# Performance work log

Hardware: AMD Instinct MI355X
Metric: run time of the kernel (lower is better)

Reference implementation:

```python
import jax, jax.numpy as jnp
import numpy as np

N = 4096
NEG_SLOPE = 0.2


def _gat_layer(x, src, dst, W, Wb, a, ab):
    # h = Linear(x); e_ij = a([h_i, h_j]) for each edge; dense softmax over dim=1; ELU
    h = x @ W + Wb                               # [N, D]
    D = h.shape[-1]
    e = h[src] @ a[:D] + h[dst] @ a[D:] + ab     # [E] per-edge attention logits
    n = x.shape[0]
    attn = jnp.full((n, n), -jnp.inf, dtype=x.dtype).at[src, dst].set(e)
    attn = jnp.where(attn > 0, attn, NEG_SLOPE * attn)   # leaky_relu (keeps -inf)
    attn = jax.nn.softmax(attn, axis=1)
    return jax.nn.elu(attn @ h)                  # sigma = ELU


def _multihead(x, src, dst, hW, hWb, ha, hab, oW, oWb, oa, oab):
    # concat=False: mean over head outputs, then out GATLayer
    heads = jax.vmap(lambda W, Wb, a, ab: _gat_layer(x, src, dst, W, Wb, a, ab))(hW, hWb, ha, hab)
    xm = heads.mean(axis=0)
    return _gat_layer(xm, src, dst, oW, oWb, oa, oab)


def setup_inputs() -> dict:
    key = jax.random.key(0)
    ks = jax.random.split(key, 20)
    in_dim, hid, out_dim, H, E = 512, 256, 128, 4, 131072
    x = jax.random.normal(ks[0], (N, in_dim), jnp.float32)
    edge_index = jax.random.randint(ks[1], (2, E), 0, N)
    # force self loops so every softmax row has at least one finite entry
    edge_index = edge_index.at[:, :N].set(jnp.broadcast_to(jnp.arange(N), (2, N)))

    def lin(k, shape, fan_in):
        return jax.random.uniform(k, shape, jnp.float32, -1.0, 1.0) / np.sqrt(fan_in).astype(np.float32)

    return {
        "x": x,
        "edge_index": edge_index,
        # layer 0 (MultiHeadGAT in_dim->hid)
        "l0_hW": lin(ks[2], (H, in_dim, hid), in_dim),
        "l0_hWb": lin(ks[3], (H, hid), in_dim),
        "l0_ha": lin(ks[4], (H, 2 * hid), 2 * hid),
        "l0_hab": lin(ks[5], (H,), 2 * hid),
        "l0_oW": lin(ks[6], (hid, hid), hid),
        "l0_oWb": lin(ks[7], (hid,), hid),
        "l0_oa": lin(ks[8], (2 * hid,), 2 * hid),
        "l0_oab": lin(ks[9], (), 2 * hid),
        # layer 1 (MultiHeadGAT hid->hid)
        "l1_hW": lin(ks[10], (H, hid, hid), hid),
        "l1_hWb": lin(ks[11], (H, hid), hid),
        "l1_ha": lin(ks[12], (H, 2 * hid), 2 * hid),
        "l1_hab": lin(ks[13], (H,), 2 * hid),
        "l1_oW": lin(ks[14], (hid, hid), hid),
        "l1_oWb": lin(ks[15], (hid,), hid),
        "l1_oa": lin(ks[16], (2 * hid,), 2 * hid),
        "l1_oab": lin(ks[17], (), 2 * hid),
        # final Linear(hid -> out_dim)
        "lin_W": lin(ks[18], (hid, out_dim), hid),
        "lin_b": lin(ks[19], (out_dim,), hid),
    }


def reference(x, edge_index, l0_hW, l0_hWb, l0_ha, l0_hab, l0_oW, l0_oWb, l0_oa, l0_oab,
              l1_hW, l1_hWb, l1_ha, l1_hab, l1_oW, l1_oWb, l1_oa, l1_oab, lin_W, lin_b):
    src, dst = edge_index[0], edge_index[1]
    lrelu = lambda v: jnp.where(v > 0, v, NEG_SLOPE * v)
    h = lrelu(_multihead(x, src, dst, l0_hW, l0_hWb, l0_ha, l0_hab, l0_oW, l0_oWb, l0_oa, l0_oab))
    h = lrelu(_multihead(h, src, dst, l1_hW, l1_hWb, l1_ha, l1_hab, l1_oW, l1_oWb, l1_oa, l1_oab))
    return h @ lin_W + lin_b  # [N, out_dim], flatten(1) is a no-op for 2D
```

## Files before the change

kernel.cpp:

```cpp
#include <hip/hip_runtime.h>
#include <hip/hip_bf16.h>
#include <math.h>

#define NEG_SLOPE 0.2f

constexpr int D = 256;
constexpr int HEADS = 4;
constexpr int MAXB = 128;

typedef __attribute__((ext_vector_type(8))) short short8;
typedef __attribute__((ext_vector_type(4))) float floatx4;

__device__ inline unsigned short bf16_hi_trunc(float v) {
  return (unsigned short)(__float_as_uint(v) >> 16);
}
__device__ inline float bf16_tof(unsigned short u) {
  return __uint_as_float(((unsigned int)u) << 16);
}
__device__ inline unsigned short bf16_rn(float v) {
  unsigned int b = __float_as_uint(v);
  b += 0x7fffu + ((b >> 16) & 1u);
  return (unsigned short)(b >> 16);
}
__device__ inline void split2(float v, unsigned short& hi, unsigned short& lo) {
  hi = bf16_hi_trunc(v);
  lo = bf16_rn(v - bf16_tof(hi));
}

__global__ void fill_kernel(const int* __restrict__ src, const int* __restrict__ dst,
                            int* __restrict__ cnt, int* __restrict__ colb, int E) {
  int k = blockIdx.x * blockDim.x + threadIdx.x;
  if (k < E) {
    int s = src[k];
    int pos = atomicAdd(&cnt[s], 1);
    if (pos < MAXB) colb[s * MAXB + pos] = dst[k];
  }
}

__global__ __launch_bounds__(128) void dedupe_kernel(const int* __restrict__ cnt,
                                                     int* __restrict__ colb, int Nn) {
  __shared__ int cs[MAXB];
  int i = blockIdx.x;
  int len = cnt[i];
  if (len > MAXB) len = MAXB;
  int tid = threadIdx.x;
  if (tid < len) cs[tid] = colb[i * MAXB + tid];
  __syncthreads();
  if (tid < len) {
    int c = cs[tid];
    bool dup = false;
    for (int s2 = 0; s2 < tid; ++s2)
      if (cs[s2] == c) { dup = true; break; }
    if (dup) colb[i * MAXB + tid] = -1;
  }
}

__global__ __launch_bounds__(256) void prep_kernel(
    int* __restrict__ zeroBase, int zeroN,
    const float* __restrict__ x, unsigned short* __restrict__ xhi, unsigned short* __restrict__ xlo,
    int xN4,
    const float* __restrict__ l0hW, unsigned short* __restrict__ l0hHi, unsigned short* __restrict__ l0hLo,
    const float* __restrict__ l1hW, unsigned short* __restrict__ l1hHi, unsigned short* __restrict__ l1hLo,
    const float* __restrict__ l0oW, unsigned short* __restrict__ l0oHi, unsigned short* __restrict__ l0oLo,
    const float* __restrict__ l1oW, unsigned short* __restrict__ l1oHi, unsigned short* __restrict__ l1oLo,
    const float* __restrict__ linW, unsigned short* __restrict__ linHi, unsigned short* __restrict__ linLo) {
  const int b = blockIdx.x;
  const int t = threadIdx.x;
  if (b < 528) {
    int idx = b * 256 + t;
    if (idx < zeroN) zeroBase[idx] = 0;
    return;
  }
  if (b < 2576) {
    int idx = (b - 528) * 256 + t;
    if (idx < xN4) {
      float4 v = ((const float4*)x)[idx];
      ushort4 h, l;
      split2(v.x, h.x, l.x);
      split2(v.y, h.y, l.y);
      split2(v.z, h.z, l.z);
      split2(v.w, h.w, l.w);
      ((ushort4*)xhi)[idx] = h;
      ((ushort4*)xlo)[idx] = l;
    }
    return;
  }
  __shared__ float tile[32][33];
  const int tr = t >> 5, tc = t & 31;
  if (b < 3088) {
    const int bi = b - 2576;
    const int kb = bi & 15;
    const int nb = (bi >> 4) & 7;
    const int h = bi >> 7;
    const int K = 512, N = 256;
    const int k0 = kb * 32, n0 = nb * 32;
    const float* B = l0hW + (size_t)h * K * N;
#pragma unroll
    for (int i = 0; i < 4; ++i)
      tile[tr + 8 * i][tc] = B[(size_t)(k0 + tr + 8 * i) * N + (n0 + tc)];
    __syncthreads();
    unsigned short* Thi = l0hHi + (size_t)h * N * K;
    unsigned short* Tlo = l0hLo + (size_t)h * N * K;
#pragma unroll
    for (int i = 0; i < 4; ++i) {
      int n = n0 + tr + 8 * i, k = k0 + tc;
      float v = tile[tc][tr + 8 * i];
      unsigned short hi, lo;
      split2(v, hi, lo);
      Thi[(size_t)n * K + k] = hi;
      Tlo[(size_t)n * K + k] = lo;
    }
    return;
  }
  const int bi = b - 3088;
  const int kb = bi & 7;
  const int nb = (bi >> 3) & 7;
  const int z = bi >> 6;
  const int K = 256;
  const int N = (z == 6) ? 128 : 256;
  const int k0 = kb * 32, n0 = nb * 32;
  if (n0 >= N) return;
  const float* B;
  unsigned short *Thi, *Tlo;
  if (z < 4) {
    B = l1hW + (size_t)z * K * 256;
    Thi = l1hHi + (size_t)z * 256 * K;
    Tlo = l1hLo + (size_t)z * 256 * K;
  } else if (z == 4) { B = l0oW; Thi = l0oHi; Tlo = l0oLo; }
  else if (z == 5)   { B = l1oW; Thi = l1oHi; Tlo = l1oLo; }
  else               { B = linW; Thi = linHi; Tlo = linLo; }
#pragma unroll
  for (int i = 0; i < 4; ++i)
    tile[tr + 8 * i][tc] = B[(size_t)(k0 + tr + 8 * i) * N + (n0 + tc)];
  __syncthreads();
#pragma unroll
  for (int i = 0; i < 4; ++i) {
    int n = n0 + tr + 8 * i, k = k0 + tc;
    float v = tile[tc][tr + 8 * i];
    unsigned short hi, lo;
    split2(v, hi, lo);
    Thi[(size_t)n * K + k] = hi;
    Tlo[(size_t)n * K + k] = lo;
  }
}

__global__ __launch_bounds__(256) void gemm_mfma_split(
    const unsigned short* __restrict__ Ahi, const unsigned short* __restrict__ Alo,
    const unsigned short* __restrict__ Ahsep, size_t planeStride,
    const unsigned short* __restrict__ Bthi, const unsigned short* __restrict__ Btlo,
    const float* __restrict__ bias, float* __restrict__ C, unsigned short* __restrict__ Cb,
    const float* __restrict__ aptr, float* __restrict__ alphaB, float* __restrict__ betaB,
    int M, int N, int K) {
  constexpr int LSTR = 72;
  __shared__ unsigned short sA[2][64 * LSTR];
  __shared__ unsigned short sB[2][64 * LSTR];
  const int tid = threadIdx.x;
  const int bm = blockIdx.x * 64;
  const int gn = blockIdx.y * 64;
  const int head = (gn) / N;
  const int bn = gn - head * N;

  const int lane = tid & 63;
  const int wv = tid >> 6;
  const int wm = (wv & 1) * 32;
  const int wn = (wv >> 1) * 32;
  const int q = lane >> 4;
  const int l15 = lane & 15;

  floatx4 acc[2][2];
#pragma unroll
  for (int i = 0; i < 2; ++i)
#pragma unroll
    for (int j = 0; j < 2; ++j) acc[i][j] = (floatx4)0.0f;

  for (int k0 = 0; k0 < K; k0 += 64) {
    short8 ra[2][2], rb[2][2];
#pragma unroll
    for (int i = 0; i < 2; ++i) {
      const int c = tid + 256 * i;
      const int row = c >> 3, koff = (c & 7) << 3;
      const size_t boff = (size_t)(gn + row) * K + k0 + koff;
      rb[0][i] = *(const short8*)(Bthi + boff);
      rb[1][i] = *(const short8*)(Btlo + boff);
      if (Ahsep) {
        const size_t aoff = (size_t)(bm + row) * K + k0 + koff;
        const short8 u0 = *(const short8*)(Ahsep + aoff);
        const short8 u1 = *(const short8*)(Ahsep + planeStride + aoff);
        const short8 u2 = *(const short8*)(Ahsep + 2 * planeStride + aoff);
        const short8 u3 = *(const short8*)(Ahsep + 3 * planeStride + aoff);
#pragma unroll
        for (int e = 0; e < 8; ++e) {
          float f = 0.25f * (bf16_tof((unsigned short)u0[e]) + bf16_tof((unsigned short)u1[e]) +
                             bf16_tof((unsigned short)u2[e]) + bf16_tof((unsigned short)u3[e]));
          unsigned short hi, lo;
          split2(f, hi, lo);
          ra[0][i][e] = (short)hi;
          ra[1][i][e] = (short)lo;
        }
      } else {
        const size_t aoff = (size_t)(bm + row) * K + k0 + koff;
        ra[0][i] = *(const short8*)(Ahi + aoff);
        ra[1][i] = *(const short8*)(Alo + aoff);
      }
    }
    __syncthreads();
#pragma unroll
    for (int i = 0; i < 2; ++i) {
      const int c = tid + 256 * i;
      const int row = c >> 3, koff = (c & 7) << 3;
      *(short8*)(&sA[0][row * LSTR + koff]) = ra[0][i];
      *(short8*)(&sA[1][row * LSTR + koff]) = ra[1][i];
      *(short8*)(&sB[0][row * LSTR + koff]) = rb[0][i];
      *(short8*)(&sB[1][row * LSTR + koff]) = rb[1][i];
    }
    __syncthreads();
#pragma unroll
    for (int kc = 0; kc < 2; ++kc) {
      const int ko = kc * 32 + q * 8;
      short8 aH[2], aL[2], bH[2], bL[2];
#pragma unroll
      for (int i = 0; i < 2; ++i) {
        aH[i] = *(const short8*)(&sA[0][(wm + i * 16 + l15) * LSTR + ko]);
        aL[i] = *(const short8*)(&sA[1][(wm + i * 16 + l15) * LSTR + ko]);
        bH[i] = *(const short8*)(&sB[0][(wn + i * 16 + l15) * LSTR + ko]);
        bL[i] = *(const short8*)(&sB[1][(wn + i * 16 + l15) * LSTR + ko]);
      }
#pragma unroll
      for (int i = 0; i < 2; ++i)
#pragma unroll
        for (int j = 0; j < 2; ++j) {
          acc[i][j] = __builtin_amdgcn_mfma_f32_16x16x32_bf16(aH[i], bH[j], acc[i][j], 0, 0, 0);
          acc[i][j] = __builtin_amdgcn_mfma_f32_16x16x32_bf16(aH[i], bL[j], acc[i][j], 0, 0, 0);
          acc[i][j] = __builtin_amdgcn_mfma_f32_16x16x32_bf16(aL[i], bH[j], acc[i][j], 0, 0, 0);
        }
    }
  }
  const size_t cBase = (size_t)head * M * N;
  const int colh0 = bn + wn + l15;
  const int colh1 = colh0 + 16;
  const float bv0 = bias[head * N + colh0];
  const float bv1 = bias[head * N + colh1];
  float as0 = 0.f, as1 = 0.f, ad0 = 0.f, ad1 = 0.f;
  if (aptr) {
    as0 = aptr[head * 2 * N + colh0];
    as1 = aptr[head * 2 * N + colh1];
    ad0 = aptr[head * 2 * N + N + colh0];
    ad1 = aptr[head * 2 * N + N + colh1];
  }
#pragma unroll
  for (int i = 0; i < 2; ++i) {
    const int rowb = bm + wm + i * 16 + q * 4;
#pragma unroll
    for (int r = 0; r < 4; ++r) {
      const float o0 = acc[i][0][r] + bv0;
      const float o1 = acc[i][1][r] + bv1;
      if (Cb) {
        Cb[cBase + (size_t)(rowb + r) * N + colh0] = bf16_rn(o0);
        Cb[cBase + (size_t)(rowb + r) * N + colh1] = bf16_rn(o1);
      } else {
        C[cBase + (size_t)(rowb + r) * N + colh0] = o0;
        C[cBase + (size_t)(rowb + r) * N + colh1] = o1;
      }
      if (aptr) {
        float pa = o0 * as0 + o1 * as1;
        float pb = o0 * ad0 + o1 * ad1;
#pragma unroll
        for (int off = 1; off < 16; off <<= 1) {
          pa += __shfl_xor(pa, off, 64);
          pb += __shfl_xor(pb, off, 64);
        }
        if (l15 == 0) {
          atomicAdd(&alphaB[head * M + rowb + r], pa);
          atomicAdd(&betaB[head * M + rowb + r], pb);
        }
      }
    }
  }
}

__global__ __launch_bounds__(256) void gemm_bias(
    const float* __restrict__ A, const float* __restrict__ B,
    const float* __restrict__ bias, float* __restrict__ C,
    int M, int N, int K) {
  __shared__ float As[16][68];
  __shared__ float Bs[16][68];
  const int tid = threadIdx.x;
  const int bm = blockIdx.x * 64;
  const int gn = blockIdx.y * 64;
  const int head = gn / N;
  const int bn = gn - head * N;
  const float* Bh = B + (size_t)head * K * N;

  const int tx = tid & 15;
  const int ty = tid >> 4;
  const int am = tid >> 2;
  const int ak = (tid & 3) << 2;
  const int bk = tid >> 4;
  const int bn4 = (tid & 15) << 2;

  float acc[4][4] = {};

  for (int k0 = 0; k0 < K; k0 += 16) {
    float4 av = *(const float4*)(A + (size_t)(bm + am) * K + (k0 + ak));
    float4 bv = *(const float4*)(Bh + (size_t)(k0 + bk) * N + (bn + bn4));
    __syncthreads();
    As[ak + 0][am] = av.x;
    As[ak + 1][am] = av.y;
    As[ak + 2][am] = av.z;
    As[ak + 3][am] = av.w;
    *(float4*)(&Bs[bk][bn4]) = bv;
    __syncthreads();
#pragma unroll
    for (int k = 0; k < 16; ++k) {
      float4 aa = *(const float4*)(&As[k][ty << 2]);
      float4 bb = *(const float4*)(&Bs[k][tx << 2]);
      acc[0][0] += aa.x * bb.x; acc[0][1] += aa.x * bb.y; acc[0][2] += aa.x * bb.z; acc[0][3] += aa.x * bb.w;
      acc[1][0] += aa.y * bb.x; acc[1][1] += aa.y * bb.y; acc[1][2] += aa.y * bb.z; acc[1][3] += aa.y * bb.w;
      acc[2][0] += aa.z * bb.x; acc[2][1] += aa.z * bb.y; acc[2][2] += aa.z * bb.z; acc[2][3] += aa.z * bb.w;
      acc[3][0] += aa.w * bb.x; acc[3][1] += aa.w * bb.y; acc[3][2] += aa.w * bb.z; acc[3][3] += aa.w * bb.w;
    }
  }
  float* Ch = C + (size_t)head * M * N;
  const float* bh = bias + (size_t)head * N;
  const int ccol = bn + (tx << 2);
  float4 bias4 = *(const float4*)(bh + ccol);
#pragma unroll
  for (int r = 0; r < 4; ++r) {
    int row = bm + (ty << 2) + r;
    float4 o;
    o.x = acc[r][0] + bias4.x;
    o.y = acc[r][1] + bias4.y;
    o.z = acc[r][2] + bias4.z;
    o.w = acc[r][3] + bias4.w;
    *(float4*)(Ch + (size_t)row * N + ccol) = o;
  }
}

__global__ __launch_bounds__(256) void alphabeta_kernel(
    const float* __restrict__ h, const float* __restrict__ a,
    float* __restrict__ alpha, float* __restrict__ beta, int Nn) {
  __shared__ float reda[4], redb[4];
  const int i = blockIdx.x;
  const int hh = blockIdx.y;
  const int tid = threadIdx.x;
  const int lane = tid & 63, wid = tid >> 6;
  float v = h[((size_t)hh * Nn + i) * D + tid];
  float pa = v * a[hh * 2 * D + tid];
  float pb = v * a[hh * 2 * D + D + tid];
#pragma unroll
  for (int off = 32; off > 0; off >>= 1) {
    pa += __shfl_xor(pa, off, 64);
    pb += __shfl_xor(pb, off, 64);
  }
  if (lane == 0) { reda[wid] = pa; redb[wid] = pb; }
  __syncthreads();
  if (tid == 0) {
    alpha[hh * Nn + i] = reda[0] + reda[1] + reda[2] + reda[3];
    beta[hh * Nn + i] = redb[0] + redb[1] + redb[2] + redb[3];
  }
}

template <int BF16H>
__global__ __launch_bounds__(256) void attn2(
    const float* __restrict__ h, const unsigned short* __restrict__ hB,
    const float* __restrict__ alpha, const float* __restrict__ beta,
    const float* __restrict__ ab, const int* __restrict__ cnt,
    const int* __restrict__ colb, float* __restrict__ out,
    unsigned short* __restrict__ oHi, unsigned short* __restrict__ oLo,
    int Nn, int H, int mode) {
  const int tid = threadIdx.x;
  const int lane = tid & 63;
  const int wv = tid >> 6;
  const int bx = blockIdx.x;
  const int head = bx % H;
  const int rowblk = bx / H;
  const int i = rowblk * 4 + wv;

  const float* hL = BF16H ? nullptr : (h + (size_t)head * Nn * D + (lane << 2));
  const unsigned short* hLB = BF16H ? (hB + (size_t)head * Nn * D + (lane << 2)) : nullptr;
  const float* betaH = beta + (size_t)head * Nn;
  const float ai = alpha[head * Nn + i] + ab[head];
  const int start = i * MAXB;
  int len = cnt[i];
  if (len > MAXB) len = MAXB;

  float m = -3.0e38f, s = 0.0f;
  float4 acc0 = make_float4(0.0f, 0.0f, 0.0f, 0.0f);
  float4 acc1 = make_float4(0.0f, 0.0f, 0.0f, 0.0f);

  for (int t0 = 0; t0 < len; t0 += 64) {
    const int t = t0 + lane;
    const int c = (t < len) ? colb[start + t] : -1;
    float e = -3.0e38f;
    if (c >= 0) {
      e = ai + betaH[c];
      e = e > 0.0f ? e : NEG_SLOPE * e;
    }
    float cm = e;
#pragma unroll
    for (int off = 32; off > 0; off >>= 1) cm = fmaxf(cm, __shfl_xor(cm, off, 64));
    const float newm = fmaxf(m, cm);
    const float scale = __expf(m - newm);
    const float w = (c >= 0) ? __expf(e - newm) : 0.0f;
    float cs = w;
#pragma unroll
    for (int off = 32; off > 0; off >>= 1) cs += __shfl_xor(cs, off, 64);
    s = s * scale + cs;
    acc0.x *= scale; acc0.y *= scale; acc0.z *= scale; acc0.w *= scale;
    acc1.x *= scale; acc1.y *= scale; acc1.z *= scale; acc1.w *= scale;
    m = newm;

    const int cS = (c >= 0) ? c : 0;
    const int cnt2 = min(64, len - t0);
    int j = 0;
    if constexpr (BF16H) {
      for (; j + 4 <= cnt2; j += 4) {
        const int c0 = __shfl(cS, j);     const float w0 = __shfl(w, j);
        const int c1 = __shfl(cS, j + 1); const float w1 = __shfl(w, j + 1);
        const int c2 = __shfl(cS, j + 2); const float w2 = __shfl(w, j + 2);
        const int c3 = __shfl(cS, j + 3); const float w3 = __shfl(w, j + 3);
        const ushort4 u0 = *(const ushort4*)(hLB + (size_t)c0 * D);
        const ushort4 u1 = *(const ushort4*)(hLB + (size_t)c1 * D);
        const ushort4 u2 = *(const ushort4*)(hLB + (size_t)c2 * D);
        const ushort4 u3 = *(const ushort4*)(hLB + (size_t)c3 * D);
        acc0.x += w0 * bf16_tof(u0.x); acc0.y += w0 * bf16_tof(u0.y);
        acc0.z += w0 * bf16_tof(u0.z); acc0.w += w0 * bf16_tof(u0.w);
        acc1.x += w1 * bf16_tof(u1.x); acc1.y += w1 * bf16_tof(u1.y);
        acc1.z += w1 * bf16_tof(u1.z); acc1.w += w1 * bf16_tof(u1.w);
        acc0.x += w2 * bf16_tof(u2.x); acc0.y += w2 * bf16_tof(u2.y);
        acc0.z += w2 * bf16_tof(u2.z); acc0.w += w2 * bf16_tof(u2.w);
        acc1.x += w3 * bf16_tof(u3.x); acc1.y += w3 * bf16_tof(u3.y);
        acc1.z += w3 * bf16_tof(u3.z); acc1.w += w3 * bf16_tof(u3.w);
      }
      for (; j < cnt2; ++j) {
        const int cj = __shfl(cS, j);
        const float wj = __shfl(w, j);
        const ushort4 u = *(const ushort4*)(hLB + (size_t)cj * D);
        acc0.x += wj * bf16_tof(u.x); acc0.y += wj * bf16_tof(u.y);
        acc0.z += wj * bf16_tof(u.z); acc0.w += wj * bf16_tof(u.w);
      }
    } else {
      for (; j + 4 <= cnt2; j += 4) {
        const int c0 = __shfl(cS, j);     const float w0 = __shfl(w, j);
        const int c1 = __shfl(cS, j + 1); const float w1 = __shfl(w, j + 1);
        const int c2 = __shfl(cS, j + 2); const float w2 = __shfl(w, j + 2);
        const int c3 = __shfl(cS, j + 3); const float w3 = __shfl(w, j + 3);
        const float4 h0 = *(const float4*)(hL + (size_t)c0 * D);
        const float4 h1 = *(const float4*)(hL + (size_t)c1 * D);
        const float4 h2 = *(const float4*)(hL + (size_t)c2 * D);
        const float4 h3 = *(const float4*)(hL + (size_t)c3 * D);
        acc0.x += w0 * h0.x; acc0.y += w0 * h0.y; acc0.z += w0 * h0.z; acc0.w += w0 * h0.w;
        acc1.x += w1 * h1.x; acc1.y += w1 * h1.y; acc1.z += w1 * h1.z; acc1.w += w1 * h1.w;
        acc0.x += w2 * h2.x; acc0.y += w2 * h2.y; acc0.z += w2 * h2.z; acc0.w += w2 * h2.w;
        acc1.x += w3 * h3.x; acc1.y += w3 * h3.y; acc1.z += w3 * h3.z; acc1.w += w3 * h3.w;
      }
      for (; j < cnt2; ++j) {
        const int cj = __shfl(cS, j);
        const float wj = __shfl(w, j);
        const float4 hv = *(const float4*)(hL + (size_t)cj * D);
        acc0.x += wj * hv.x; acc0.y += wj * hv.y;
        acc0.z += wj * hv.z; acc0.w += wj * hv.w;
      }
    }
  }

  const float inv = 1.0f / s;
  float4 v;
  v.x = (acc0.x + acc1.x) * inv; v.y = (acc0.y + acc1.y) * inv;
  v.z = (acc0.z + acc1.z) * inv; v.w = (acc0.w + acc1.w) * inv;
  v.x = v.x > 0.0f ? v.x : expm1f(v.x);
  v.y = v.y > 0.0f ? v.y : expm1f(v.y);
  v.z = v.z > 0.0f ? v.z : expm1f(v.z);
  v.w = v.w > 0.0f ? v.w : expm1f(v.w);

  if (mode == 1 || mode == 3) {
    v.x = v.x > 0.0f ? v.x : NEG_SLOPE * v.x;
    v.y = v.y > 0.0f ? v.y : NEG_SLOPE * v.y;
    v.z = v.z > 0.0f ? v.z : NEG_SLOPE * v.z;
    v.w = v.w > 0.0f ? v.w : NEG_SLOPE * v.w;
    if (mode == 1) {
      *(float4*)(out + (size_t)i * D + (lane << 2)) = v;
    } else {
      ushort4 h4, l4;
      split2(v.x, h4.x, l4.x);
      split2(v.y, h4.y, l4.y);
      split2(v.z, h4.z, l4.z);
      split2(v.w, h4.w, l4.w);
      const size_t q4 = ((size_t)i * D >> 2) + lane;
      ((ushort4*)oHi)[q4] = h4;
      ((ushort4*)oLo)[q4] = l4;
    }
  } else if (mode == 0) {
    if constexpr (BF16H) {
      ushort4 h4;
      h4.x = bf16_rn(v.x);
      h4.y = bf16_rn(v.y);
      h4.z = bf16_rn(v.z);
      h4.w = bf16_rn(v.w);
      const size_t q4 = (((size_t)head * Nn + i) * D >> 2) + lane;
      ((ushort4*)oHi)[q4] = h4;
    } else {
      *(float4*)(out + ((size_t)head * Nn + i) * D + (lane << 2)) = v;
    }
  } else {
    const float invH = 1.0f / (float)H;
    float* o = out + (size_t)i * D + (lane << 2);
    atomicAdd(o + 0, invH * v.x);
    atomicAdd(o + 1, invH * v.y);
    atomicAdd(o + 2, invH * v.z);
    atomicAdd(o + 3, invH * v.w);
  }
}

__global__ __launch_bounds__(256) void mean4_kernel(
    float* __restrict__ hsep, int total4) {
  int idx = blockIdx.x * blockDim.x + threadIdx.x;
  if (idx < total4) {
    float4* p = (float4*)hsep;
    float4 a = p[idx], b = p[idx + total4], c = p[idx + 2 * total4], d = p[idx + 3 * total4];
    float4 o;
    o.x = 0.25f * (a.x + b.x + c.x + d.x);
    o.y = 0.25f * (a.y + b.y + c.y + d.y);
    o.z = 0.25f * (a.z + b.z + c.z + d.z);
    o.w = 0.25f * (a.w + b.w + c.w + d.w);
    p[idx] = o;
  }
}

__global__ void zero_ints(int* __restrict__ p, int n) {
  int i = blockIdx.x * blockDim.x + threadIdx.x;
  if (i < n) p[i] = 0;
}

__global__ void zero_floats(float* __restrict__ p, int n) {
  int i = blockIdx.x * blockDim.x + threadIdx.x;
  if (i < n) p[i] = 0.0f;
}

extern "C" void kernel_launch(void* const* d_in, const int* in_sizes, int n_in,
                              void* d_out, int out_size, void* d_ws, size_t ws_size,
                              hipStream_t stream) {
  const float* x = (const float*)d_in[0];
  const int* eidx = (const int*)d_in[1];
  const float* l0_hW = (const float*)d_in[2];
  const float* l0_hWb = (const float*)d_in[3];
  const float* l0_ha = (const float*)d_in[4];
  const float* l0_hab = (const float*)d_in[5];
  const float* l0_oW = (const float*)d_in[6];
  const float* l0_oWb = (const float*)d_in[7];
  const float* l0_oa = (const float*)d_in[8];
  const float* l0_oab = (const float*)d_in[9];
  const float* l1_hW = (const float*)d_in[10];
  const float* l1_hWb = (const float*)d_in[11];
  const float* l1_ha = (const float*)d_in[12];
  const float* l1_hab = (const float*)d_in[13];
  const float* l1_oW = (const float*)d_in[14];
  const float* l1_oWb = (const float*)d_in[15];
  const float* l1_oa = (const float*)d_in[16];
  const float* l1_oab = (const float*)d_in[17];
  const float* lin_W = (const float*)d_in[18];
  const float* lin_b = (const float*)d_in[19];

  const int in_dim = 512;
  const int Nn = in_sizes[0] / in_dim;
  const int E = in_sizes[1] / 2;
  const int out_dim = 128;

  char* wsp = (char*)d_ws;
  auto alloc = [&](size_t bytes) {
    char* p = wsp;
    wsp += (bytes + 255) & ~(size_t)255;
    return p;
  };
  const size_t ndBytes = sizeof(float) * (size_t)Nn * D;
  const size_t mfmaNeed = 52000000;
  const bool mfma = ws_size >= mfmaNeed;

  if (mfma) {
    unsigned short* hbufB = (unsigned short*)alloc((size_t)HEADS * Nn * D * 2);
    unsigned short* houtB = (unsigned short*)alloc((size_t)Nn * D * 2);
    unsigned short* hsepB = (unsigned short*)alloc((size_t)HEADS * Nn * D * 2);
    unsigned short* xhi  = (unsigned short*)alloc((size_t)Nn * in_dim * 2);
    unsigned short* xlo  = (unsigned short*)alloc((size_t)Nn * in_dim * 2);
    unsigned short* x1hi = xhi;
    unsigned short* x1lo = xlo;
    unsigned short* l0hHi = (unsigned short*)alloc((size_t)HEADS * in_dim * D * 2);
    unsigned short* l0hLo = (unsigned short*)alloc((size_t)HEADS * in_dim * D * 2);
    unsigned short* l1hHi = (unsigned short*)alloc((size_t)HEADS * D * D * 2);
    unsigned short* l1hLo = (unsigned short*)alloc((size_t)HEADS * D * D * 2);
    unsigned short* l0oHi = (unsigned short*)alloc((size_t)D * D * 2);
    unsigned short* l0oLo = (unsigned short*)alloc((size_t)D * D * 2);
    unsigned short* l1oHi = (unsigned short*)alloc((size_t)D * D * 2);
    unsigned short* l1oLo = (unsigned short*)alloc((size_t)D * D * 2);
    unsigned short* linHi = (unsigned short*)alloc((size_t)D * out_dim * 2);
    unsigned short* linLo = (unsigned short*)alloc((size_t)D * out_dim * 2);
    int* cnt     = (int*)alloc(sizeof(int) * Nn);
    float* abz   = (float*)alloc(sizeof(float) * 4 * 2 * HEADS * (size_t)Nn);
    int* colb    = (int*)alloc(sizeof(int) * (size_t)Nn * MAXB);
    auto alphaS = [&](int s) { return abz + (size_t)s * 2 * HEADS * Nn; };
    auto betaS  = [&](int s) { return abz + (size_t)s * 2 * HEADS * Nn + HEADS * Nn; };

    const int* src = eidx;
    const int* dst = eidx + E;

    const int zeroN = Nn + 4 * 2 * HEADS * Nn;
    prep_kernel<<<3536, 256, 0, stream>>>(
        cnt, zeroN,
        x, xhi, xlo, Nn * in_dim / 4,
        l0_hW, l0hHi, l0hLo, l1_hW, l1hHi, l1hLo,
        l0_oW, l0oHi, l0oLo, l1_oW, l1oHi, l1oLo, lin_W, linHi, linLo);

    fill_kernel<<<(E + 255) / 256, 256, 0, stream>>>(src, dst, cnt, colb, E);
    dedupe_kernel<<<Nn, 128, 0, stream>>>(cnt, colb, Nn);

    const size_t pStride = (size_t)Nn * D;

    gemm_mfma_split<<<dim3(Nn / 64, HEADS * D / 64), 256, 0, stream>>>(
        xhi, xlo, nullptr, 0, l0hHi, l0hLo, l0_hWb, nullptr, hbufB,
        l0_ha, alphaS(0), betaS(0), Nn, D, in_dim);
    attn2<1><<<HEADS * (Nn / 4), 256, 0, stream>>>(nullptr, hbufB, alphaS(0), betaS(0), l0_hab,
                                                   cnt, colb, nullptr, hsepB, nullptr, Nn, HEADS, 0);
    gemm_mfma_split<<<dim3(Nn / 64, D / 64), 256, 0, stream>>>(
        nullptr, nullptr, hsepB, pStride, l0oHi, l0oLo, l0_oWb, nullptr, houtB,
        l0_oa, alphaS(1), betaS(1), Nn, D, D);
    attn2<1><<<Nn / 4, 256, 0, stream>>>(nullptr, houtB, alphaS(1), betaS(1), l0_oab,
                                         cnt, colb, nullptr, x1hi, x1lo, Nn, 1, 3);

    gemm_mfma_split<<<dim3(Nn / 64, HEADS * D / 64), 256, 0, stream>>>(
        x1hi, x1lo, nullptr, 0, l1hHi, l1hLo, l1_hWb, nullptr, hbufB,
        l1_ha, alphaS(2), betaS(2), Nn, D, D);
    attn2<1><<<HEADS * (Nn / 4), 256, 0, stream>>>(nullptr, hbufB, alphaS(2), betaS(2), l1_hab,
                                                   cnt, colb, nullptr, hsepB, nullptr, Nn, HEADS, 0);
    gemm_mfma_split<<<dim3(Nn / 64, D / 64), 256, 0, stream>>>(
        nullptr, nullptr, hsepB, pStride, l1oHi, l1oLo, l1_oWb, nullptr, houtB,
        l1_oa, alphaS(3), betaS(3), Nn, D, D);
    attn2<1><<<Nn / 4, 256, 0, stream>>>(nullptr, houtB, alphaS(3), betaS(3), l1_oab,
                                         cnt, colb, nullptr, x1hi, x1lo, Nn, 1, 3);

    gemm_mfma_split<<<dim3(Nn / 64, out_dim / 64), 256, 0, stream>>>(
        x1hi, x1lo, nullptr, 0, linHi, linLo, lin_b, (float*)d_out, nullptr,
        nullptr, nullptr, nullptr, Nn, out_dim, D);
    return;
  }

  const size_t smallBytes = sizeof(float) * 2 * HEADS * (size_t)Nn + sizeof(int) * (Nn + (size_t)Nn * MAXB) + 4096;
  const bool staged = ws_size >= (8 * ndBytes + 2 * ndBytes + smallBytes + 65536);

  float* hbuf  = (float*)alloc(ndBytes * HEADS);
  float* hsep  = staged ? (float*)alloc(ndBytes * HEADS) : nullptr;
  float* xm    = staged ? hsep : (float*)alloc(ndBytes);
  float* x1    = (float*)alloc(ndBytes);
  float* hout  = (float*)alloc(ndBytes);
  float* alpha = (float*)alloc(sizeof(float) * HEADS * (size_t)Nn);
  float* beta  = (float*)alloc(sizeof(float) * HEADS * (size_t)Nn);
  int* cnt     = (int*)alloc(sizeof(int) * Nn);
  int* colb    = (int*)alloc(sizeof(int) * (size_t)Nn * MAXB);

  const int* src = eidx;
  const int* dst = eidx + E;

  zero_ints<<<(Nn + 255) / 256, 256, 0, stream>>>(cnt, Nn);
  fill_kernel<<<(E + 255) / 256, 256, 0, stream>>>(src, dst, cnt, colb, E);
  dedupe_kernel<<<Nn, 128, 0, stream>>>(cnt, colb, Nn);

  const int total4 = Nn * D / 4;
  const int meanBlocks = (total4 + 255) / 256;

  gemm_bias<<<dim3(Nn / 64, HEADS * D / 64), 256, 0, stream>>>(x, l0_hW, l0_hWb, hbuf, Nn, D, in_dim);
  alphabeta_kernel<<<dim3(Nn, HEADS), 256, 0, stream>>>(hbuf, l0_ha, alpha, beta, Nn);
  if (staged) {
    attn2<0><<<HEADS * (Nn / 4), 256, 0, stream>>>(hbuf, nullptr, alpha, beta, l0_hab, cnt, colb, hsep, nullptr, nullptr, Nn, HEADS, 0);
    mean4_kernel<<<meanBlocks, 256, 0, stream>>>(hsep, total4);
  } else {
    zero_floats<<<(Nn * D + 255) / 256, 256, 0, stream>>>(xm, Nn * D);
    attn2<0><<<HEADS * (Nn / 4), 256, 0, stream>>>(hbuf, nullptr, alpha, beta, l0_hab, cnt, colb, xm, nullptr, nullptr, Nn, HEADS, 2);
  }
  gemm_bias<<<dim3(Nn / 64, D / 64), 256, 0, stream>>>(xm, l0_oW, l0_oWb, hout, Nn, D, D);
  alphabeta_kernel<<<dim3(Nn, 1), 256, 0, stream>>>(hout, l0_oa, alpha, beta, Nn);
  attn2<0><<<Nn / 4, 256, 0, stream>>>(hout, nullptr, alpha, beta, l0_oab, cnt, colb, x1, nullptr, nullptr, Nn, 1, 1);

  gemm_bias<<<dim3(Nn / 64, HEADS * D / 64), 256, 0, stream>>>(x1, l1_hW, l1_hWb, hbuf, Nn, D, D);
  alphabeta_kernel<<<dim3(Nn, HEADS), 256, 0, stream>>>(hbuf, l1_ha, alpha, beta, Nn);
  if (staged) {
    attn2<0><<<HEADS * (Nn / 4), 256, 0, stream>>>(hbuf, nullptr, alpha, beta, l1_hab, cnt, colb, hsep, nullptr, nullptr, Nn, HEADS, 0);
    mean4_kernel<<<meanBlocks, 256, 0, stream>>>(hsep, total4);
  } else {
    zero_floats<<<(Nn * D + 255) / 256, 256, 0, stream>>>(xm, Nn * D);
    attn2<0><<<HEADS * (Nn / 4), 256, 0, stream>>>(hbuf, nullptr, alpha, beta, l1_hab, cnt, colb, xm, nullptr, nullptr, Nn, HEADS, 2);
  }
  gemm_bias<<<dim3(Nn / 64, D / 64), 256, 0, stream>>>(xm, l1_oW, l1_oWb, hout, Nn, D, D);
  alphabeta_kernel<<<dim3(Nn, 1), 256, 0, stream>>>(hout, l1_oa, alpha, beta, Nn);
  attn2<0><<<Nn / 4, 256, 0, stream>>>(hout, nullptr, alpha, beta, l1_oab, cnt, colb, x1, nullptr, nullptr, Nn, 1, 1);

  gemm_bias<<<dim3(Nn / 64, out_dim / 64), 256, 0, stream>>>(x1, lin_W, lin_b, (float*)d_out, Nn, out_dim, D);
}
```

Baseline: 252.4 us.

## Fuse four-head attention aggregation with head-mean into one kernel using interleaved layout

Changes the head GEMM output to a node-major interleaved layout ([N, H, D]) with alpha/beta stored per node across heads. A new attn4 kernel handles all four heads per node in one pass: it loads each neighbor's four head rows together, runs an online softmax per head, applies ELU, averages the heads and writes the hi/lo split result directly. This removes the per-head separate output buffer and the 4-plane mean-and-split work inside the following GEMM's A-load, and shares neighbor index and beta loads across heads. The cost is more registers per thread in attn4 and a fixed dependence on HEADS being 4.

```diff
diff --git a/kernel.cpp b/kernel.cpp
--- a/kernel.cpp
+++ b/kernel.cpp
@@ -146,7 +146,6 @@
 
 __global__ __launch_bounds__(256) void gemm_mfma_split(
     const unsigned short* __restrict__ Ahi, const unsigned short* __restrict__ Alo,
-    const unsigned short* __restrict__ Ahsep, size_t planeStride,
     const unsigned short* __restrict__ Bthi, const unsigned short* __restrict__ Btlo,
     const float* __restrict__ bias, float* __restrict__ C, unsigned short* __restrict__ Cb,
     const float* __restrict__ aptr, float* __restrict__ alphaB, float* __restrict__ betaB,
@@ -159,6 +158,7 @@
   const int gn = blockIdx.y * 64;
   const int head = (gn) / N;
   const int bn = gn - head * N;
+  const int Htot = (int)((gridDim.y * 64) / N);
 
   const int lane = tid & 63;
   const int wv = tid >> 6;
@@ -182,26 +182,9 @@
       const size_t boff = (size_t)(gn + row) * K + k0 + koff;
       rb[0][i] = *(const short8*)(Bthi + boff);
       rb[1][i] = *(const short8*)(Btlo + boff);
-      if (Ahsep) {
-        const size_t aoff = (size_t)(bm + row) * K + k0 + koff;
-        const short8 u0 = *(const short8*)(Ahsep + aoff);
-        const short8 u1 = *(const short8*)(Ahsep + planeStride + aoff);
-        const short8 u2 = *(const short8*)(Ahsep + 2 * planeStride + aoff);
-        const short8 u3 = *(const short8*)(Ahsep + 3 * planeStride + aoff);
-#pragma unroll
-        for (int e = 0; e < 8; ++e) {
-          float f = 0.25f * (bf16_tof((unsigned short)u0[e]) + bf16_tof((unsigned short)u1[e]) +
-                             bf16_tof((unsigned short)u2[e]) + bf16_tof((unsigned short)u3[e]));
-          unsigned short hi, lo;
-          split2(f, hi, lo);
-          ra[0][i][e] = (short)hi;
-          ra[1][i][e] = (short)lo;
-        }
-      } else {
-        const size_t aoff = (size_t)(bm + row) * K + k0 + koff;
-        ra[0][i] = *(const short8*)(Ahi + aoff);
-        ra[1][i] = *(const short8*)(Alo + aoff);
-      }
+      const size_t aoff = (size_t)(bm + row) * K + k0 + koff;
+      ra[0][i] = *(const short8*)(Ahi + aoff);
+      ra[1][i] = *(const short8*)(Alo + aoff);
     }
     __syncthreads();
 #pragma unroll
@@ -235,7 +218,8 @@
         }
     }
   }
-  const size_t cBase = (size_t)head * M * N;
+  const size_t rowStride = (size_t)Htot * N;
+  const size_t headOff = (size_t)head * N;
   const int colh0 = bn + wn + l15;
   const int colh1 = colh0 + 16;
   const float bv0 = bias[head * N + colh0];
@@ -255,11 +239,11 @@
       const float o0 = acc[i][0][r] + bv0;
       const float o1 = acc[i][1][r] + bv1;
       if (Cb) {
-        Cb[cBase + (size_t)(rowb + r) * N + colh0] = bf16_rn(o0);
-        Cb[cBase + (size_t)(rowb + r) * N + colh1] = bf16_rn(o1);
+        Cb[(size_t)(rowb + r) * rowStride + headOff + colh0] = bf16_rn(o0);
+        Cb[(size_t)(rowb + r) * rowStride + headOff + colh1] = bf16_rn(o1);
       } else {
-        C[cBase + (size_t)(rowb + r) * N + colh0] = o0;
-        C[cBase + (size_t)(rowb + r) * N + colh1] = o1;
+        C[(size_t)(rowb + r) * N + colh0] = o0;
+        C[(size_t)(rowb + r) * N + colh1] = o1;
       }
       if (aptr) {
         float pa = o0 * as0 + o1 * as1;
@@ -270,8 +254,8 @@
           pb += __shfl_xor(pb, off, 64);
         }
         if (l15 == 0) {
-          atomicAdd(&alphaB[head * M + rowb + r], pa);
-          atomicAdd(&betaB[head * M + rowb + r], pb);
+          atomicAdd(&alphaB[(size_t)(rowb + r) * Htot + head], pa);
+          atomicAdd(&betaB[(size_t)(rowb + r) * Htot + head], pb);
         }
       }
     }
@@ -358,6 +342,152 @@
     alpha[hh * Nn + i] = reda[0] + reda[1] + reda[2] + reda[3];
     beta[hh * Nn + i] = redb[0] + redb[1] + redb[2] + redb[3];
   }
+}
+
+__global__ __launch_bounds__(256) void attn4(
+    const unsigned short* __restrict__ hB,
+    const float* __restrict__ alpha, const float* __restrict__ beta,
+    const float* __restrict__ ab, const int* __restrict__ cnt,
+    const int* __restrict__ colb,
+    unsigned short* __restrict__ oHi, unsigned short* __restrict__ oLo, int Nn) {
+  const int tid = threadIdx.x;
+  const int lane = tid & 63;
+  const int wv = tid >> 6;
+  const int i = blockIdx.x * 4 + wv;
+
+  const unsigned short* hL = hB + (lane << 2);
+  const float ai0 = alpha[i * HEADS + 0] + ab[0];
+  const float ai1 = alpha[i * HEADS + 1] + ab[1];
+  const float ai2 = alpha[i * HEADS + 2] + ab[2];
+  const float ai3 = alpha[i * HEADS + 3] + ab[3];
+  const int start = i * MAXB;
+  int len = cnt[i];
+  if (len > MAXB) len = MAXB;
+
+  float m0 = -3.0e38f, m1 = -3.0e38f, m2 = -3.0e38f, m3 = -3.0e38f;
+  float s0 = 0.f, s1 = 0.f, s2 = 0.f, s3 = 0.f;
+  float4 A0 = make_float4(0.f, 0.f, 0.f, 0.f);
+  float4 A1 = make_float4(0.f, 0.f, 0.f, 0.f);
+  float4 A2 = make_float4(0.f, 0.f, 0.f, 0.f);
+  float4 A3 = make_float4(0.f, 0.f, 0.f, 0.f);
+
+  for (int t0 = 0; t0 < len; t0 += 64) {
+    const int t = t0 + lane;
+    const int c = (t < len) ? colb[start + t] : -1;
+    float e0 = -3.0e38f, e1 = -3.0e38f, e2 = -3.0e38f, e3 = -3.0e38f;
+    if (c >= 0) {
+      const float4 b4 = *(const float4*)(beta + (size_t)c * HEADS);
+      e0 = ai0 + b4.x; e1 = ai1 + b4.y; e2 = ai2 + b4.z; e3 = ai3 + b4.w;
+      e0 = e0 > 0.0f ? e0 : NEG_SLOPE * e0;
+      e1 = e1 > 0.0f ? e1 : NEG_SLOPE * e1;
+      e2 = e2 > 0.0f ? e2 : NEG_SLOPE * e2;
+      e3 = e3 > 0.0f ? e3 : NEG_SLOPE * e3;
+    }
+    float c0 = e0, c1 = e1, c2 = e2, c3 = e3;
+#pragma unroll
+    for (int off = 32; off > 0; off >>= 1) {
+      c0 = fmaxf(c0, __shfl_xor(c0, off, 64));
+      c1 = fmaxf(c1, __shfl_xor(c1, off, 64));
+      c2 = fmaxf(c2, __shfl_xor(c2, off, 64));
+      c3 = fmaxf(c3, __shfl_xor(c3, off, 64));
+    }
+    const float n0 = fmaxf(m0, c0), n1 = fmaxf(m1, c1);
+    const float n2 = fmaxf(m2, c2), n3 = fmaxf(m3, c3);
+    const float sc0 = __expf(m0 - n0), sc1 = __expf(m1 - n1);
+    const float sc2 = __expf(m2 - n2), sc3 = __expf(m3 - n3);
+    float w0 = 0.f, w1 = 0.f, w2 = 0.f, w3 = 0.f;
+    if (c >= 0) {
+      w0 = __expf(e0 - n0); w1 = __expf(e1 - n1);
+      w2 = __expf(e2 - n2); w3 = __expf(e3 - n3);
+    }
+    float q0 = w0, q1 = w1, q2 = w2, q3 = w3;
+#pragma unroll
+    for (int off = 32; off > 0; off >>= 1) {
+      q0 += __shfl_xor(q0, off, 64);
+      q1 += __shfl_xor(q1, off, 64);
+      q2 += __shfl_xor(q2, off, 64);
+      q3 += __shfl_xor(q3, off, 64);
+    }
+    s0 = s0 * sc0 + q0; s1 = s1 * sc1 + q1;
+    s2 = s2 * sc2 + q2; s3 = s3 * sc3 + q3;
+    A0.x *= sc0; A0.y *= sc0; A0.z *= sc0; A0.w *= sc0;
+    A1.x *= sc1; A1.y *= sc1; A1.z *= sc1; A1.w *= sc1;
+    A2.x *= sc2; A2.y *= sc2; A2.z *= sc2; A2.w *= sc2;
+    A3.x *= sc3; A3.y *= sc3; A3.z *= sc3; A3.w *= sc3;
+    m0 = n0; m1 = n1; m2 = n2; m3 = n3;
+
+    const int cS = (c >= 0) ? c : 0;
+    const int cnt2 = min(64, len - t0);
+    int j = 0;
+    for (; j + 2 <= cnt2; j += 2) {
+      const int ca = __shfl(cS, j);
+      const int cb = __shfl(cS, j + 1);
+      const float wa0 = __shfl(w0, j),     wa1 = __shfl(w1, j);
+      const float wa2 = __shfl(w2, j),     wa3 = __shfl(w3, j);
+      const float wb0 = __shfl(w0, j + 1), wb1 = __shfl(w1, j + 1);
+      const float wb2 = __shfl(w2, j + 1), wb3 = __shfl(w3, j + 1);
+      const unsigned short* pa = hL + (size_t)ca * (HEADS * D);
+      const unsigned short* pb = hL + (size_t)cb * (HEADS * D);
+      const ushort4 ua0 = *(const ushort4*)(pa);
+      const ushort4 ua1 = *(const ushort4*)(pa + D);
+      const ushort4 ua2 = *(const ushort4*)(pa + 2 * D);
+      const ushort4 ua3 = *(const ushort4*)(pa + 3 * D);
+      const ushort4 ub0 = *(const ushort4*)(pb);
+      const ushort4 ub1 = *(const ushort4*)(pb + D);
+      const ushort4 ub2 = *(const ushort4*)(pb + 2 * D);
+      const ushort4 ub3 = *(const ushort4*)(pb + 3 * D);
+      A0.x += wa0 * bf16_tof(ua0.x); A0.y += wa0 * bf16_tof(ua0.y);
+      A0.z += wa0 * bf16_tof(ua0.z); A0.w += wa0 * bf16_tof(ua0.w);
+      A1.x += wa1 * bf16_tof(ua1.x); A1.y += wa1 * bf16_tof(ua1.y);
+      A1.z += wa1 * bf16_tof(ua1.z); A1.w += wa1 * bf16_tof(ua1.w);
+      A2.x += wa2 * bf16_tof(ua2.x); A2.y += wa2 * bf16_tof(ua2.y);
+      A2.z += wa2 * bf16_tof(ua2.z); A2.w += wa2 * bf16_tof(ua2.w);
+      A3.x += wa3 * bf16_tof(ua3.x); A3.y += wa3 * bf16_tof(ua3.y);
+      A3.z += wa3 * bf16_tof(ua3.z); A3.w += wa3 * bf16_tof(ua3.w);
+      A0.x += wb0 * bf16_tof(ub0.x); A0.y += wb0 * bf16_tof(ub0.y);
+      A0.z += wb0 * bf16_tof(ub0.z); A0.w += wb0 * bf16_tof(ub0.w);
+      A1.x += wb1 * bf16_tof(ub1.x); A1.y += wb1 * bf16_tof(ub1.y);
+      A1.z += wb1 * bf16_tof(ub1.z); A1.w += wb1 * bf16_tof(ub1.w);
+      A2.x += wb2 * bf16_tof(ub2.x); A2.y += wb2 * bf16_tof(ub2.y);
+      A2.z += wb2 * bf16_tof(ub2.z); A2.w += wb2 * bf16_tof(ub2.w);
+      A3.x += wb3 * bf16_tof(ub3.x); A3.y += wb3 * bf16_tof(ub3.y);
+      A3.z += wb3 * bf16_tof(ub3.z); A3.w += wb3 * bf16_tof(ub3.w);
+    }
+    for (; j < cnt2; ++j) {
+      const int ca = __shfl(cS, j);
+      const float wa0 = __shfl(w0, j), wa1 = __shfl(w1, j);
+      const float wa2 = __shfl(w2, j), wa3 = __shfl(w3, j);
+      const unsigned short* pa = hL + (size_t)ca * (HEADS * D);
+      const ushort4 ua0 = *(const ushort4*)(pa);
+      const ushort4 ua1 = *(const ushort4*)(pa + D);
+      const ushort4 ua2 = *(const ushort4*)(pa + 2 * D);
+      const ushort4 ua3 = *(const ushort4*)(pa + 3 * D);
+      A0.x += wa0 * bf16_tof(ua0.x); A0.y += wa0 * bf16_tof(ua0.y);
+      A0.z += wa0 * bf16_tof(ua0.z); A0.w += wa0 * bf16_tof(ua0.w);
+      A1.x += wa1 * bf16_tof(ua1.x); A1.y += wa1 * bf16_tof(ua1.y);
+      A1.z += wa1 * bf16_tof(ua1.z); A1.w += wa1 * bf16_tof(ua1.w);
+      A2.x += wa2 * bf16_tof(ua2.x); A2.y += wa2 * bf16_tof(ua2.y);
+      A2.z += wa2 * bf16_tof(ua2.z); A2.w += wa2 * bf16_tof(ua2.w);
+      A3.x += wa3 * bf16_tof(ua3.x); A3.y += wa3 * bf16_tof(ua3.y);
+      A3.z += wa3 * bf16_tof(ua3.z); A3.w += wa3 * bf16_tof(ua3.w);
+    }
+  }
+
+  const float i0 = 1.0f / s0, i1 = 1.0f / s1, i2 = 1.0f / s2, i3 = 1.0f / s3;
+  auto elu = [](float x) { return x > 0.0f ? x : expm1f(x); };
+  float4 xm;
+  xm.x = 0.25f * (elu(A0.x * i0) + elu(A1.x * i1) + elu(A2.x * i2) + elu(A3.x * i3));
+  xm.y = 0.25f * (elu(A0.y * i0) + elu(A1.y * i1) + elu(A2.y * i2) + elu(A3.y * i3));
+  xm.z = 0.25f * (elu(A0.z * i0) + elu(A1.z * i1) + elu(A2.z * i2) + elu(A3.z * i3));
+  xm.w = 0.25f * (elu(A0.w * i0) + elu(A1.w * i1) + elu(A2.w * i2) + elu(A3.w * i3));
+  ushort4 h4, l4;
+  split2(xm.x, h4.x, l4.x);
+  split2(xm.y, h4.y, l4.y);
+  split2(xm.z, h4.z, l4.z);
+  split2(xm.w, h4.w, l4.w);
+  const size_t q4 = ((size_t)i * D >> 2) + lane;
+  ((ushort4*)oHi)[q4] = h4;
+  ((ushort4*)oLo)[q4] = l4;
 }
 
 template <int BF16H>
@@ -579,7 +709,8 @@
   if (mfma) {
     unsigned short* hbufB = (unsigned short*)alloc((size_t)HEADS * Nn * D * 2);
     unsigned short* houtB = (unsigned short*)alloc((size_t)Nn * D * 2);
-    unsigned short* hsepB = (unsigned short*)alloc((size_t)HEADS * Nn * D * 2);
+    unsigned short* xmHi  = (unsigned short*)alloc((size_t)Nn * D * 2);
+    unsigned short* xmLo  = (unsigned short*)alloc((size_t)Nn * D * 2);
     unsigned short* xhi  = (unsigned short*)alloc((size_t)Nn * in_dim * 2);
     unsigned short* xlo  = (unsigned short*)alloc((size_t)Nn * in_dim * 2);
     unsigned short* x1hi = xhi;
@@ -613,32 +744,30 @@
     fill_kernel<<<(E + 255) / 256, 256, 0, stream>>>(src, dst, cnt, colb, E);
     dedupe_kernel<<<Nn, 128, 0, stream>>>(cnt, colb, Nn);
 
-    const size_t pStride = (size_t)Nn * D;
-
     gemm_mfma_split<<<dim3(Nn / 64, HEADS * D / 64), 256, 0, stream>>>(
-        xhi, xlo, nullptr, 0, l0hHi, l0hLo, l0_hWb, nullptr, hbufB,
+        xhi, xlo, l0hHi, l0hLo, l0_hWb, nullptr, hbufB,
         l0_ha, alphaS(0), betaS(0), Nn, D, in_dim);
-    attn2<1><<<HEADS * (Nn / 4), 256, 0, stream>>>(nullptr, hbufB, alphaS(0), betaS(0), l0_hab,
-                                                   cnt, colb, nullptr, hsepB, nullptr, Nn, HEADS, 0);
+    attn4<<<Nn / 4, 256, 0, stream>>>(hbufB, alphaS(0), betaS(0), l0_hab,
+                                      cnt, colb, xmHi, xmLo, Nn);
     gemm_mfma_split<<<dim3(Nn / 64, D / 64), 256, 0, stream>>>(
-        nullptr, nullptr, hsepB, pStride, l0oHi, l0oLo, l0_oWb, nullptr, houtB,
+        xmHi, xmLo, l0oHi, l0oLo, l0_oWb, nullptr, houtB,
         l0_oa, alphaS(1), betaS(1), Nn, D, D);
     attn2<1><<<Nn / 4, 256, 0, stream>>>(nullptr, houtB, alphaS(1), betaS(1), l0_oab,
                                          cnt, colb, nullptr, x1hi, x1lo, Nn, 1, 3);
 
     gemm_mfma_split<<<dim3(Nn / 64, HEADS * D / 64), 256, 0, stream>>>(
-        x1hi, x1lo, nullptr, 0, l1hHi, l1hLo, l1_hWb, nullptr, hbufB,
+        x1hi, x1lo, l1hHi, l1hLo, l1_hWb, nullptr, hbufB,
         l1_ha, alphaS(2), betaS(2), Nn, D, D);
-    attn2<1><<<HEADS * (Nn / 4), 256, 0, stream>>>(nullptr, hbufB, alphaS(2), betaS(2), l1_hab,
-                                                   cnt, colb, nullptr, hsepB, nullptr, Nn, HEADS, 0);
+    attn4<<<Nn / 4, 256, 0, stream>>>(hbufB, alphaS(2), betaS(2), l1_hab,
+                                      cnt, colb, xmHi, xmLo, Nn);
     gemm_mfma_split<<<dim3(Nn / 64, D / 64), 256, 0, stream>>>(
-        nullptr, nullptr, hsepB, pStride, l1oHi, l1oLo, l1_oWb, nullptr, houtB,
+        xmHi, xmLo, l1oHi, l1oLo, l1_oWb, nullptr, houtB,
         l1_oa, alphaS(3), betaS(3), Nn, D, D);
     attn2<1><<<Nn / 4, 256, 0, stream>>>(nullptr, houtB, alphaS(3), betaS(3), l1_oab,
                                          cnt, colb, nullptr, x1hi, x1lo, Nn, 1, 3);
 
     gemm_mfma_split<<<dim3(Nn / 64, out_dim / 64), 256, 0, stream>>>(
-        x1hi, x1lo, nullptr, 0, linHi, linLo, lin_b, (float*)d_out, nullptr,
+        x1hi, x1lo, linHi, linLo, lin_b, (float*)d_out, nullptr,
         nullptr, nullptr, nullptr, Nn, out_dim, D);
     return;
   }
```

Result: slower. 272.7 us (+8.0%).
